# Kernel tuning notes

Hardware: AMD Instinct MI355X
Metric: run time of the kernel (lower is better)

Reference implementation:

```python
import jax, jax.numpy as jnp
import numpy as np

T, H, I, E, K = 4096, 2048, 1408, 8, 2  # tokens, hidden, intermediate, experts, top_k


def setup_inputs() -> dict:
    key = jax.random.key(0)
    ks = jax.random.split(key, 6)
    hidden_states = jax.random.normal(ks[0], (T, H), dtype=jnp.float32)
    gate_weight = jax.random.normal(ks[1], (E, H), dtype=jnp.float32) * 0.02  # fp32 gate, per source assert
    w13_weight = jax.random.randint(ks[2], (E, 2 * I, H), -127, 128, dtype=jnp.int8)
    w13_weight_scale = jax.random.uniform(ks[3], (E, 2 * I), dtype=jnp.float32, minval=0.5, maxval=1.5) * 0.005
    w2_weight = jax.random.randint(ks[4], (E, H, I), -127, 128, dtype=jnp.int8)
    w2_weight_scale = jax.random.uniform(ks[5], (E, H), dtype=jnp.float32, minval=0.5, maxval=1.5) * 0.005
    return dict(hidden_states=hidden_states, gate_weight=gate_weight,
                w13_weight=w13_weight, w13_weight_scale=w13_weight_scale,
                w2_weight=w2_weight, w2_weight_scale=w2_weight_scale)


def _dynamic_quant_i8(x):
    # per-token dynamic symmetric int8: scale = max|x|/127 (smooth scales default to ones)
    s = jnp.maximum(jnp.max(jnp.abs(x), axis=-1, keepdims=True) / 127.0, 1e-8)
    q = jnp.clip(jnp.round(x / s), -127.0, 127.0)
    return q, s


def reference(hidden_states, gate_weight, w13_weight, w13_weight_scale, w2_weight, w2_weight_scale):
    # --- gating: fp32 linear + topk softmax (renormalize=True) ---
    logits = hidden_states @ gate_weight.T              # [T, E]
    probs = jax.nn.softmax(logits, axis=-1)
    topv, topi = jax.lax.top_k(probs, K)                # [T, K]
    gates = topv / jnp.sum(topv, axis=-1, keepdims=True)
    # dense routing weights [T, E]: gate value where expert selected, else 0
    route = jnp.zeros((T, E), hidden_states.dtype).at[jnp.arange(T)[:, None], topi].add(gates)

    # --- dynamic per-token int8 quant of routed input (same token value for each of its K copies) ---
    q_in, s_in = _dynamic_quant_i8(hidden_states)       # [T, H], [T, 1]

    # --- grouped w8a8 GEMM (fc1) -> SwiGLU -> requant -> grouped GEMM (fc2) -> weighted combine ---
    def step(acc, xs):
        w13, s13, w2, s2w, r = xs                       # per-expert weights / route column [T]
        h1 = (q_in @ w13.T.astype(jnp.float32)) * s_in * s13[None, :]   # dequant fc1: [T, 2I]
        g, u = h1[:, :I], h1[:, I:]
        act = jax.nn.silu(g) * u                        # SwiGLU
        q_a, s_a = _dynamic_quant_i8(act)
        h2 = (q_a @ w2.T.astype(jnp.float32)) * s_a * s2w[None, :]      # dequant fc2: [T, H]
        return acc + r[:, None] * h2, None

    acc0 = jnp.zeros_like(hidden_states)
    out, _ = jax.lax.scan(step, acc0,
                          (w13_weight, w13_weight_scale, w2_weight, w2_weight_scale, route.T))
    return out
```

## Files before the change

kernel.cpp:

```cpp
#include <hip/hip_runtime.h>

#define T_TOK 4096
#define H_DIM 2048
#define I_DIM 1408
#define E_NUM 8
#define NI2   (2 * I_DIM)

typedef int v4i __attribute__((ext_vector_type(4)));

#define GLD_LDS16(gptr, lptr)                                                        \
  __builtin_amdgcn_global_load_lds(                                                  \
      (const __attribute__((address_space(1))) void*)(gptr),                         \
      (__attribute__((address_space(3))) void*)(lptr), 16, 0, 0)

__global__ __launch_bounds__(256) void pack_all(const int* __restrict__ w13,
                                                const int* __restrict__ w2,
                                                signed char* __restrict__ qw13,
                                                signed char* __restrict__ qw2,
                                                int n16a, int n16tot) {
  int i = blockIdx.x * 256 + threadIdx.x;
  if (i >= n16tot) return;
  const int* src;
  signed char* dst;
  int j;
  if (i < n16a) { src = w13; dst = qw13; j = i; }
  else          { src = w2;  dst = qw2;  j = i - n16a; }
  const int4* s4 = (const int4*)src + (size_t)j * 4;
  int4 v0 = s4[0], v1 = s4[1], v2 = s4[2], v3 = s4[3];
  union { signed char c[16]; int4 v; } pk;
  pk.c[0] = (signed char)v0.x;  pk.c[1] = (signed char)v0.y;
  pk.c[2] = (signed char)v0.z;  pk.c[3] = (signed char)v0.w;
  pk.c[4] = (signed char)v1.x;  pk.c[5] = (signed char)v1.y;
  pk.c[6] = (signed char)v1.z;  pk.c[7] = (signed char)v1.w;
  pk.c[8] = (signed char)v2.x;  pk.c[9] = (signed char)v2.y;
  pk.c[10] = (signed char)v2.z; pk.c[11] = (signed char)v2.w;
  pk.c[12] = (signed char)v3.x; pk.c[13] = (signed char)v3.y;
  pk.c[14] = (signed char)v3.z; pk.c[15] = (signed char)v3.w;
  ((int4*)dst)[j] = pk.v;
}

__global__ __launch_bounds__(256) void gate_route_quant(
    const float* __restrict__ hs, const float* __restrict__ gw,
    signed char* __restrict__ qin, float* __restrict__ s_in,
    int* __restrict__ tope, float* __restrict__ gts) {
  const int t = blockIdx.x;
  const int tid = threadIdx.x;
  const int lane = tid & 63;
  const int wave = tid >> 6;
  const float* row = hs + (size_t)t * H_DIM;

  const float4* r4 = (const float4*)row + tid * 2;
  float4 xa = r4[0], xb = r4[1];
  float x[8] = {xa.x, xa.y, xa.z, xa.w, xb.x, xb.y, xb.z, xb.w};

  double pd[8];
  for (int e = 0; e < 8; e++) pd[e] = 0.0;
  float am = 0.f;
  for (int j = 0; j < 8; j++) {
    float v = x[j];
    am = fmaxf(am, fabsf(v));
    int col = tid * 8 + j;
    for (int e = 0; e < 8; e++)
      pd[e] += (double)v * (double)gw[e * H_DIM + col];
  }
  for (int e = 0; e < 8; e++)
    for (int s = 32; s; s >>= 1) pd[e] += __shfl_down(pd[e], s);
  for (int s = 32; s; s >>= 1) am = fmaxf(am, __shfl_down(am, s));

  __shared__ double sred[4][8];
  __shared__ float sam[4];
  __shared__ float sbc;
  if (lane == 0) {
    for (int e = 0; e < 8; e++) sred[wave][e] = pd[e];
    sam[wave] = am;
  }
  __syncthreads();
  if (tid == 0) {
    float l[8];
    for (int e = 0; e < 8; e++)
      l[e] = (float)(sred[0][e] + sred[1][e] + sred[2][e] + sred[3][e]);
    float amx = fmaxf(fmaxf(sam[0], sam[1]), fmaxf(sam[2], sam[3]));
    float s = fmaxf(amx / 127.0f, 1e-8f);
    s_in[t] = s;
    sbc = s;
    int i1 = 0;
    for (int e = 1; e < 8; e++) if (l[e] > l[i1]) i1 = e;
    int i2 = -1;
    for (int e = 0; e < 8; e++) {
      if (e == i1) continue;
      if (i2 < 0 || l[e] > l[i2]) i2 = e;
    }
    float d = expf(l[i2] - l[i1]);
    tope[2 * t] = i1;     gts[2 * t] = 1.0f / (1.0f + d);
    tope[2 * t + 1] = i2; gts[2 * t + 1] = d / (1.0f + d);
  }
  __syncthreads();
  float s = sbc;
  union { signed char c[8]; unsigned long long u; } pk;
  for (int j = 0; j < 8; j++) {
    float q = rintf(x[j] / s);
    q = fminf(127.f, fmaxf(-127.f, q));
    pk.c[j] = (signed char)q;
  }
  ((unsigned long long*)(qin + (size_t)t * H_DIM))[tid] = pk.u;
}

__global__ __launch_bounds__(256) void build_lists(
    const int* __restrict__ tope, int* __restrict__ tok_list,
    int* __restrict__ epos, int* __restrict__ cnt) {
  const int e = blockIdx.x;
  const int tid = threadIdx.x;
  const int lane = tid & 63;
  const int wave = tid >> 6;
  __shared__ int wsum[4];
  __shared__ int base_s;
  if (tid == 0) base_s = 0;
  __syncthreads();
  for (int t0 = 0; t0 < T_TOK; t0 += 256) {
    int t = t0 + tid;
    int i1 = tope[2 * t], i2 = tope[2 * t + 1];
    int slot = (i1 == e) ? 0 : ((i2 == e) ? 1 : -1);
    unsigned long long m = __ballot(slot >= 0);
    int wpre = __popcll(m & ((1ull << lane) - 1ull));
    if (lane == 0) wsum[wave] = __popcll(m);
    __syncthreads();
    int pre = wpre;
    for (int w = 0; w < wave; w++) pre += wsum[w];
    int total = wsum[0] + wsum[1] + wsum[2] + wsum[3];
    int b = base_s;
    if (slot >= 0) {
      int pos = b + pre;
      tok_list[e * T_TOK + pos] = t;
      epos[2 * t + slot] = (e << 16) | pos;
    }
    __syncthreads();
    if (tid == 0) base_s = b + total;
  }
  __syncthreads();
  if (tid == 0) cnt[e] = base_s;
}

__global__ void calc_off(const int* __restrict__ cnt, int* __restrict__ off) {
  if (threadIdx.x == 0) {
    int s = 0;
    for (int e = 0; e < E_NUM; e++) { off[e] = s; s += cnt[e]; }
  }
}

__global__ __launch_bounds__(256, 3) void gemm1_silu(
    const signed char* __restrict__ qw13, const signed char* __restrict__ qin,
    const float* __restrict__ s_in, const float* __restrict__ s13,
    const int* __restrict__ tok_list, const int* __restrict__ cnt,
    const int* __restrict__ off, float* __restrict__ act,
    unsigned int* __restrict__ amax) {
  const int e = blockIdx.z;
  const int ce = cnt[e];
  const int m0 = blockIdx.y * 64;
  if (m0 >= ce) return;
  const int n0 = blockIdx.x * 128;

  __shared__ __align__(16) signed char As[64 * 64];
  __shared__ __align__(16) signed char Bg[128 * 64];
  __shared__ __align__(16) signed char Bu[128 * 64];

  const int tid = threadIdx.x;
  const int lane = tid & 63;
  const int wave = tid >> 6;
  const int quad = lane >> 4;
  const int ln = lane & 15;

  const int* tl = tok_list + e * T_TOK;
  const int rowA = tid >> 2;
  const int kc = (tid & 3) * 16;

  const int tA = tl[min(m0 + rowA, ce - 1)];
  const signed char* gA = qin + (size_t)tA * H_DIM + kc;
  const signed char* w13e = qw13 + (size_t)e * NI2 * H_DIM;
  const signed char* gBg0 = w13e + (size_t)(n0 + rowA) * H_DIM + kc;
  const signed char* gBg1 = w13e + (size_t)(n0 + rowA + 64) * H_DIM + kc;
  const signed char* gBu0 = gBg0 + (size_t)I_DIM * H_DIM;
  const signed char* gBu1 = gBg1 + (size_t)I_DIM * H_DIM;
  const int ldsA = tid * 16;
  const int lds1 = 4096 + ldsA;

  v4i accg[4][2], accu[4][2];
  v4i zero = {0, 0, 0, 0};
#pragma unroll
  for (int i = 0; i < 4; i++)
#pragma unroll
    for (int j = 0; j < 2; j++) { accg[i][j] = zero; accu[i][j] = zero; }

  for (int k0 = 0; k0 < H_DIM; k0 += 64) {
    __syncthreads();
    GLD_LDS16(gA + k0, As + ldsA);
    GLD_LDS16(gBg0 + k0, Bg + ldsA);
    GLD_LDS16(gBg1 + k0, Bg + lds1);
    GLD_LDS16(gBu0 + k0, Bu + ldsA);
    GLD_LDS16(gBu1 + k0, Bu + lds1);
    __syncthreads();

    v4i af[4], bgf[2], buf_[2];
#pragma unroll
    for (int mt = 0; mt < 4; mt++)
      af[mt] = *(const v4i*)(As + (mt * 16 + ln) * 64 + quad * 16);
#pragma unroll
    for (int nt = 0; nt < 2; nt++) {
      bgf[nt] = *(const v4i*)(Bg + (wave * 32 + nt * 16 + ln) * 64 + quad * 16);
      buf_[nt] = *(const v4i*)(Bu + (wave * 32 + nt * 16 + ln) * 64 + quad * 16);
    }
#pragma unroll
    for (int mt = 0; mt < 4; mt++)
#pragma unroll
      for (int nt = 0; nt < 2; nt++) {
        accg[mt][nt] = __builtin_amdgcn_mfma_i32_16x16x64_i8(af[mt], bgf[nt], accg[mt][nt], 0, 0, 0);
        accu[mt][nt] = __builtin_amdgcn_mfma_i32_16x16x64_i8(af[mt], buf_[nt], accu[mt][nt], 0, 0, 0);
      }
  }

  const float* s13e = s13 + e * NI2;
  float sg[2], su[2];
  int ncol[2];
#pragma unroll
  for (int nt = 0; nt < 2; nt++) {
    int n = n0 + wave * 32 + nt * 16 + ln;
    ncol[nt] = n;
    sg[nt] = s13e[n];
    su[nt] = s13e[I_DIM + n];
  }
  const int offe = off[e];
#pragma unroll
  for (int mt = 0; mt < 4; mt++) {
#pragma unroll
    for (int r = 0; r < 4; r++) {
      int mrel = m0 + mt * 16 + quad * 4 + r;
      bool valid = mrel < ce;
      int tok = tl[valid ? mrel : 0];
      float si = s_in[tok];
      int crow = offe + mrel;
      float* arow = act + (size_t)crow * I_DIM;
      float am = 0.f;
#pragma unroll
      for (int nt = 0; nt < 2; nt++) {
        float g = (float)accg[mt][nt][r] * si * sg[nt];
        float u = (float)accu[mt][nt][r] * si * su[nt];
        float a = g / (1.0f + expf(-g)) * u;
        if (valid) arow[ncol[nt]] = a;
        am = fmaxf(am, fabsf(a));
      }
      for (int s = 1; s < 16; s <<= 1) am = fmaxf(am, __shfl_xor(am, s, 16));
      if (valid && ln == 0) atomicMax(amax + crow, __float_as_uint(am));
    }
  }
}

__global__ __launch_bounds__(256) void quant_act(const float* __restrict__ act,
                                                 const unsigned int* __restrict__ amax,
                                                 signed char* __restrict__ qa,
                                                 float* __restrict__ s_a) {
  const int r = blockIdx.x;
  float am = __uint_as_float(amax[r]);
  float s = fmaxf(am / 127.0f, 1e-8f);
  if (threadIdx.x == 0) s_a[r] = s;
  const float* arow = act + (size_t)r * I_DIM;
  signed char* qrow = qa + (size_t)r * I_DIM;
  for (int j = threadIdx.x; j < I_DIM; j += 256) {
    float q = rintf(arow[j] / s);
    q = fminf(127.f, fmaxf(-127.f, q));
    qrow[j] = (signed char)q;
  }
}

__global__ __launch_bounds__(256, 4) void gemm2_h2(
    const signed char* __restrict__ qw2, const signed char* __restrict__ qa,
    const float* __restrict__ s_a, const float* __restrict__ s2w,
    const int* __restrict__ cnt, const int* __restrict__ off,
    float* __restrict__ h2s) {
  const int e = blockIdx.z;
  const int ce = cnt[e];
  const int m0 = blockIdx.y * 64;
  if (m0 >= ce) return;
  const int n0 = blockIdx.x * 128;
  const int offe = off[e];

  __shared__ __align__(16) signed char As[64 * 64];
  __shared__ __align__(16) signed char Bs[128 * 64];

  const int tid = threadIdx.x;
  const int lane = tid & 63;
  const int wave = tid >> 6;
  const int quad = lane >> 4;
  const int ln = lane & 15;

  const int rowA = tid >> 2;
  const int kc = (tid & 3) * 16;

  const signed char* gA = qa + (size_t)(offe + min(m0 + rowA, ce - 1)) * I_DIM + kc;
  const signed char* w2e = qw2 + (size_t)e * H_DIM * I_DIM;
  const signed char* gB0 = w2e + (size_t)(n0 + rowA) * I_DIM + kc;
  const signed char* gB1 = w2e + (size_t)(n0 + rowA + 64) * I_DIM + kc;
  const int ldsA = tid * 16;
  const int lds1 = 4096 + ldsA;

  v4i acc[4][2];
  v4i zero = {0, 0, 0, 0};
#pragma unroll
  for (int i = 0; i < 4; i++)
#pragma unroll
    for (int j = 0; j < 2; j++) acc[i][j] = zero;

  for (int k0 = 0; k0 < I_DIM; k0 += 64) {
    __syncthreads();
    GLD_LDS16(gA + k0, As + ldsA);
    GLD_LDS16(gB0 + k0, Bs + ldsA);
    GLD_LDS16(gB1 + k0, Bs + lds1);
    __syncthreads();

    v4i af[4], bf[2];
#pragma unroll
    for (int mt = 0; mt < 4; mt++)
      af[mt] = *(const v4i*)(As + (mt * 16 + ln) * 64 + quad * 16);
#pragma unroll
    for (int nt = 0; nt < 2; nt++)
      bf[nt] = *(const v4i*)(Bs + (wave * 32 + nt * 16 + ln) * 64 + quad * 16);
#pragma unroll
    for (int mt = 0; mt < 4; mt++)
#pragma unroll
      for (int nt = 0; nt < 2; nt++)
        acc[mt][nt] = __builtin_amdgcn_mfma_i32_16x16x64_i8(af[mt], bf[nt], acc[mt][nt], 0, 0, 0);
  }

  const float* s2e = s2w + e * H_DIM;
  float sw[2];
  int ncol[2];
#pragma unroll
  for (int nt = 0; nt < 2; nt++) {
    int n = n0 + wave * 32 + nt * 16 + ln;
    ncol[nt] = n;
    sw[nt] = s2e[n];
  }
#pragma unroll
  for (int mt = 0; mt < 4; mt++) {
#pragma unroll
    for (int r = 0; r < 4; r++) {
      int mrel = m0 + mt * 16 + quad * 4 + r;
      if (mrel >= ce) continue;
      float sa = s_a[offe + mrel];
      float* orow = h2s + (size_t)(offe + mrel) * H_DIM;
#pragma unroll
      for (int nt = 0; nt < 2; nt++)
        orow[ncol[nt]] = (float)acc[mt][nt][r] * sa * sw[nt];
    }
  }
}

__global__ __launch_bounds__(256) void gather_out(
    const float* __restrict__ h2s, const int* __restrict__ epos,
    const float* __restrict__ gts, const int* __restrict__ off,
    float* __restrict__ out) {
  const int t = blockIdx.x;
  int a = epos[2 * t], b = epos[2 * t + 1];
  float g1 = gts[2 * t], g2 = gts[2 * t + 1];
  int r1 = off[a >> 16] + (a & 0xffff);
  int r2 = off[b >> 16] + (b & 0xffff);
  const float4* R1 = (const float4*)(h2s + (size_t)r1 * H_DIM);
  const float4* R2 = (const float4*)(h2s + (size_t)r2 * H_DIM);
  float4* O = (float4*)(out + (size_t)t * H_DIM);
  for (int c = threadIdx.x; c < H_DIM / 4; c += 256) {
    float4 x = R1[c], y = R2[c];
    float4 z;
    z.x = g1 * x.x + g2 * y.x;
    z.y = g1 * x.y + g2 * y.y;
    z.z = g1 * x.z + g2 * y.z;
    z.w = g1 * x.w + g2 * y.w;
    O[c] = z;
  }
}

extern "C" void kernel_launch(void* const* d_in, const int* in_sizes, int n_in,
                              void* d_out, int out_size, void* d_ws, size_t ws_size,
                              hipStream_t stream) {
  const float* hs = (const float*)d_in[0];
  const float* gw = (const float*)d_in[1];
  const int* w13 = (const int*)d_in[2];
  const float* s13 = (const float*)d_in[3];
  const int* w2 = (const int*)d_in[4];
  const float* s2w = (const float*)d_in[5];
  float* out = (float*)d_out;

  char* ws = (char*)d_ws;
  size_t o = 0;
  auto take = [&](size_t b) {
    char* p = ws + o;
    o += (b + 255) & ~(size_t)255;
    return p;
  };
  signed char* qw13 = (signed char*)take((size_t)E_NUM * NI2 * H_DIM);
  signed char* qin = (signed char*)take((size_t)T_TOK * H_DIM);
  float* act = (float*)take((size_t)T_TOK * 2 * I_DIM * 4);
  float* h2s = (float*)qw13;
  signed char* qw2 = (signed char*)take((size_t)E_NUM * H_DIM * I_DIM);
  signed char* qa = (signed char*)take((size_t)T_TOK * 2 * I_DIM);
  float* sin_ = (float*)take((size_t)T_TOK * 4);
  float* sa = (float*)take((size_t)T_TOK * 2 * 4);
  unsigned int* amax = (unsigned int*)take((size_t)T_TOK * 2 * 4);
  int* tokl = (int*)take((size_t)E_NUM * T_TOK * 4);
  int* tope = (int*)take((size_t)T_TOK * 2 * 4);
  int* epos = (int*)take((size_t)T_TOK * 2 * 4);
  float* gts = (float*)take((size_t)T_TOK * 2 * 4);
  int* cnt = (int*)take(E_NUM * 4);
  int* off = (int*)take(E_NUM * 4);

  hipMemsetAsync(amax, 0, (size_t)T_TOK * 2 * 4, stream);

  {
    int n16a = E_NUM * NI2 * H_DIM / 16;
    int n16b = E_NUM * H_DIM * I_DIM / 16;
    int n16tot = n16a + n16b;
    pack_all<<<(n16tot + 255) / 256, 256, 0, stream>>>(w13, w2, qw13, qw2, n16a, n16tot);
  }
  gate_route_quant<<<T_TOK, 256, 0, stream>>>(hs, gw, qin, sin_, tope, gts);
  build_lists<<<E_NUM, 256, 0, stream>>>(tope, tokl, epos, cnt);
  calc_off<<<1, 64, 0, stream>>>(cnt, off);
  {
    dim3 g(I_DIM / 128, T_TOK / 64, E_NUM);
    gemm1_silu<<<g, 256, 0, stream>>>(qw13, qin, sin_, s13, tokl, cnt, off, act, amax);
  }
  quant_act<<<T_TOK * 2, 256, 0, stream>>>(act, amax, qa, sa);
  {
    dim3 g(H_DIM / 128, T_TOK / 64, E_NUM);
    gemm2_h2<<<g, 256, 0, stream>>>(qw2, qa, sa, s2w, cnt, off, h2s);
  }
  gather_out<<<T_TOK, 256, 0, stream>>>(h2s, epos, gts, off, out);
}
```

Before: 582.4 us.

## Double-buffer GEMM LDS tiles, swizzle LDS, widen gemm2 tile, parallelize list build

Both grouped GEMMs now double-buffer their LDS tiles, so the next k-slice's global-to-LDS loads are issued before the MFMAs on the current slice. Both also use an XOR swizzle on the LDS k-chunk to reduce bank conflicts. gemm2's N tile grows to 256 with a 4x4 accumulator set. Both GEMMs use a flattened 1D grid with the expert index in the low bits to interleave experts. build_lists now runs across 16 blocks using shared-memory and global atomics, with cnt cleared by a memset. This trades more LDS and registers per block, which may lower occupancy, and makes token order within each expert list nondeterministic.

```diff
diff --git a/kernel.cpp b/kernel.cpp
--- a/kernel.cpp
+++ b/kernel.cpp
@@ -108,36 +108,24 @@
 __global__ __launch_bounds__(256) void build_lists(
     const int* __restrict__ tope, int* __restrict__ tok_list,
     int* __restrict__ epos, int* __restrict__ cnt) {
-  const int e = blockIdx.x;
+  __shared__ int lc[E_NUM];
+  __shared__ int lbase[E_NUM];
   const int tid = threadIdx.x;
-  const int lane = tid & 63;
-  const int wave = tid >> 6;
-  __shared__ int wsum[4];
-  __shared__ int base_s;
-  if (tid == 0) base_s = 0;
-  __syncthreads();
-  for (int t0 = 0; t0 < T_TOK; t0 += 256) {
-    int t = t0 + tid;
-    int i1 = tope[2 * t], i2 = tope[2 * t + 1];
-    int slot = (i1 == e) ? 0 : ((i2 == e) ? 1 : -1);
-    unsigned long long m = __ballot(slot >= 0);
-    int wpre = __popcll(m & ((1ull << lane) - 1ull));
-    if (lane == 0) wsum[wave] = __popcll(m);
-    __syncthreads();
-    int pre = wpre;
-    for (int w = 0; w < wave; w++) pre += wsum[w];
-    int total = wsum[0] + wsum[1] + wsum[2] + wsum[3];
-    int b = base_s;
-    if (slot >= 0) {
-      int pos = b + pre;
-      tok_list[e * T_TOK + pos] = t;
-      epos[2 * t + slot] = (e << 16) | pos;
-    }
-    __syncthreads();
-    if (tid == 0) base_s = b + total;
-  }
-  __syncthreads();
-  if (tid == 0) cnt[e] = base_s;
+  if (tid < E_NUM) lc[tid] = 0;
+  __syncthreads();
+  const int t = blockIdx.x * 256 + tid;
+  int e0 = tope[2 * t], e1 = tope[2 * t + 1];
+  int p0 = atomicAdd(&lc[e0], 1);
+  int p1 = atomicAdd(&lc[e1], 1);
+  __syncthreads();
+  if (tid < E_NUM) lbase[tid] = atomicAdd(&cnt[tid], lc[tid]);
+  __syncthreads();
+  int pos0 = lbase[e0] + p0;
+  int pos1 = lbase[e1] + p1;
+  tok_list[e0 * T_TOK + pos0] = t;
+  tok_list[e1 * T_TOK + pos1] = t;
+  epos[2 * t] = (e0 << 16) | pos0;
+  epos[2 * t + 1] = (e1 << 16) | pos1;
 }
 
 __global__ void calc_off(const int* __restrict__ cnt, int* __restrict__ off) {
@@ -153,15 +141,18 @@
     const int* __restrict__ tok_list, const int* __restrict__ cnt,
     const int* __restrict__ off, float* __restrict__ act,
     unsigned int* __restrict__ amax) {
-  const int e = blockIdx.z;
+  const int bid = blockIdx.x;
+  const int e = bid & 7;
+  const int xt = bid >> 9;
+  const int yt = (bid >> 3) & 63;
   const int ce = cnt[e];
-  const int m0 = blockIdx.y * 64;
+  const int m0 = yt * 64;
   if (m0 >= ce) return;
-  const int n0 = blockIdx.x * 128;
-
-  __shared__ __align__(16) signed char As[64 * 64];
-  __shared__ __align__(16) signed char Bg[128 * 64];
-  __shared__ __align__(16) signed char Bu[128 * 64];
+  const int n0 = xt * 128;
+
+  __shared__ __align__(16) signed char As[2][64 * 64];
+  __shared__ __align__(16) signed char Bg[2][128 * 64];
+  __shared__ __align__(16) signed char Bu[2][128 * 64];
 
   const int tid = threadIdx.x;
   const int lane = tid & 63;
@@ -171,7 +162,7 @@
 
   const int* tl = tok_list + e * T_TOK;
   const int rowA = tid >> 2;
-  const int kc = (tid & 3) * 16;
+  const int kc = (((tid & 3) ^ (rowA & 3)) * 16);
 
   const int tA = tl[min(m0 + rowA, ce - 1)];
   const signed char* gA = qin + (size_t)tA * H_DIM + kc;
@@ -182,6 +173,7 @@
   const signed char* gBu1 = gBg1 + (size_t)I_DIM * H_DIM;
   const int ldsA = tid * 16;
   const int lds1 = 4096 + ldsA;
+  const int ks = ((quad ^ (ln & 3)) * 16);
 
   v4i accg[4][2], accu[4][2];
   v4i zero = {0, 0, 0, 0};
@@ -190,23 +182,32 @@
 #pragma unroll
     for (int j = 0; j < 2; j++) { accg[i][j] = zero; accu[i][j] = zero; }
 
-  for (int k0 = 0; k0 < H_DIM; k0 += 64) {
-    __syncthreads();
-    GLD_LDS16(gA + k0, As + ldsA);
-    GLD_LDS16(gBg0 + k0, Bg + ldsA);
-    GLD_LDS16(gBg1 + k0, Bg + lds1);
-    GLD_LDS16(gBu0 + k0, Bu + ldsA);
-    GLD_LDS16(gBu1 + k0, Bu + lds1);
-    __syncthreads();
-
+  GLD_LDS16(gA, &As[0][ldsA]);
+  GLD_LDS16(gBg0, &Bg[0][ldsA]);
+  GLD_LDS16(gBg1, &Bg[0][lds1]);
+  GLD_LDS16(gBu0, &Bu[0][ldsA]);
+  GLD_LDS16(gBu1, &Bu[0][lds1]);
+  __syncthreads();
+
+  const int NK = H_DIM / 64;
+  for (int kk = 0; kk < NK; ++kk) {
+    const int cur = kk & 1;
+    if (kk + 1 < NK) {
+      const int k0 = (kk + 1) * 64;
+      GLD_LDS16(gA + k0, &As[cur ^ 1][ldsA]);
+      GLD_LDS16(gBg0 + k0, &Bg[cur ^ 1][ldsA]);
+      GLD_LDS16(gBg1 + k0, &Bg[cur ^ 1][lds1]);
+      GLD_LDS16(gBu0 + k0, &Bu[cur ^ 1][ldsA]);
+      GLD_LDS16(gBu1 + k0, &Bu[cur ^ 1][lds1]);
+    }
     v4i af[4], bgf[2], buf_[2];
 #pragma unroll
     for (int mt = 0; mt < 4; mt++)
-      af[mt] = *(const v4i*)(As + (mt * 16 + ln) * 64 + quad * 16);
+      af[mt] = *(const v4i*)(&As[cur][(mt * 16 + ln) * 64 + ks]);
 #pragma unroll
     for (int nt = 0; nt < 2; nt++) {
-      bgf[nt] = *(const v4i*)(Bg + (wave * 32 + nt * 16 + ln) * 64 + quad * 16);
-      buf_[nt] = *(const v4i*)(Bu + (wave * 32 + nt * 16 + ln) * 64 + quad * 16);
+      bgf[nt] = *(const v4i*)(&Bg[cur][(wave * 32 + nt * 16 + ln) * 64 + ks]);
+      buf_[nt] = *(const v4i*)(&Bu[cur][(wave * 32 + nt * 16 + ln) * 64 + ks]);
     }
 #pragma unroll
     for (int mt = 0; mt < 4; mt++)
@@ -215,6 +216,7 @@
         accg[mt][nt] = __builtin_amdgcn_mfma_i32_16x16x64_i8(af[mt], bgf[nt], accg[mt][nt], 0, 0, 0);
         accu[mt][nt] = __builtin_amdgcn_mfma_i32_16x16x64_i8(af[mt], buf_[nt], accu[mt][nt], 0, 0, 0);
       }
+    __syncthreads();
   }
 
   const float* s13e = s13 + e * NI2;
@@ -270,20 +272,23 @@
   }
 }
 
-__global__ __launch_bounds__(256, 4) void gemm2_h2(
+__global__ __launch_bounds__(256, 3) void gemm2_h2(
     const signed char* __restrict__ qw2, const signed char* __restrict__ qa,
     const float* __restrict__ s_a, const float* __restrict__ s2w,
     const int* __restrict__ cnt, const int* __restrict__ off,
     float* __restrict__ h2s) {
-  const int e = blockIdx.z;
+  const int bid = blockIdx.x;
+  const int e = bid & 7;
+  const int xt = bid >> 9;
+  const int yt = (bid >> 3) & 63;
   const int ce = cnt[e];
-  const int m0 = blockIdx.y * 64;
+  const int m0 = yt * 64;
   if (m0 >= ce) return;
-  const int n0 = blockIdx.x * 128;
+  const int n0 = xt * 256;
   const int offe = off[e];
 
-  __shared__ __align__(16) signed char As[64 * 64];
-  __shared__ __align__(16) signed char Bs[128 * 64];
+  __shared__ __align__(16) signed char As[2][64 * 64];
+  __shared__ __align__(16) signed char Bs[2][256 * 64];
 
   const int tid = threadIdx.x;
   const int lane = tid & 63;
@@ -292,49 +297,63 @@
   const int ln = lane & 15;
 
   const int rowA = tid >> 2;
-  const int kc = (tid & 3) * 16;
+  const int kc = (((tid & 3) ^ (rowA & 3)) * 16);
 
   const signed char* gA = qa + (size_t)(offe + min(m0 + rowA, ce - 1)) * I_DIM + kc;
   const signed char* w2e = qw2 + (size_t)e * H_DIM * I_DIM;
   const signed char* gB0 = w2e + (size_t)(n0 + rowA) * I_DIM + kc;
-  const signed char* gB1 = w2e + (size_t)(n0 + rowA + 64) * I_DIM + kc;
+  const signed char* gB1 = gB0 + (size_t)64 * I_DIM;
+  const signed char* gB2 = gB0 + (size_t)128 * I_DIM;
+  const signed char* gB3 = gB0 + (size_t)192 * I_DIM;
   const int ldsA = tid * 16;
-  const int lds1 = 4096 + ldsA;
-
-  v4i acc[4][2];
+  const int ks = ((quad ^ (ln & 3)) * 16);
+
+  v4i acc[4][4];
   v4i zero = {0, 0, 0, 0};
 #pragma unroll
   for (int i = 0; i < 4; i++)
 #pragma unroll
-    for (int j = 0; j < 2; j++) acc[i][j] = zero;
-
-  for (int k0 = 0; k0 < I_DIM; k0 += 64) {
+    for (int j = 0; j < 4; j++) acc[i][j] = zero;
+
+  GLD_LDS16(gA, &As[0][ldsA]);
+  GLD_LDS16(gB0, &Bs[0][ldsA]);
+  GLD_LDS16(gB1, &Bs[0][4096 + ldsA]);
+  GLD_LDS16(gB2, &Bs[0][8192 + ldsA]);
+  GLD_LDS16(gB3, &Bs[0][12288 + ldsA]);
+  __syncthreads();
+
+  const int NK = I_DIM / 64;
+  for (int kk = 0; kk < NK; ++kk) {
+    const int cur = kk & 1;
+    if (kk + 1 < NK) {
+      const int k0 = (kk + 1) * 64;
+      GLD_LDS16(gA + k0, &As[cur ^ 1][ldsA]);
+      GLD_LDS16(gB0 + k0, &Bs[cur ^ 1][ldsA]);
+      GLD_LDS16(gB1 + k0, &Bs[cur ^ 1][4096 + ldsA]);
+      GLD_LDS16(gB2 + k0, &Bs[cur ^ 1][8192 + ldsA]);
+      GLD_LDS16(gB3 + k0, &Bs[cur ^ 1][12288 + ldsA]);
+    }
+    v4i af[4], bf[4];
+#pragma unroll
+    for (int mt = 0; mt < 4; mt++)
+      af[mt] = *(const v4i*)(&As[cur][(mt * 16 + ln) * 64 + ks]);
+#pragma unroll
+    for (int nt = 0; nt < 4; nt++)
+      bf[nt] = *(const v4i*)(&Bs[cur][(wave * 64 + nt * 16 + ln) * 64 + ks]);
+#pragma unroll
+    for (int mt = 0; mt < 4; mt++)
+#pragma unroll
+      for (int nt = 0; nt < 4; nt++)
+        acc[mt][nt] = __builtin_amdgcn_mfma_i32_16x16x64_i8(af[mt], bf[nt], acc[mt][nt], 0, 0, 0);
     __syncthreads();
-    GLD_LDS16(gA + k0, As + ldsA);
-    GLD_LDS16(gB0 + k0, Bs + ldsA);
-    GLD_LDS16(gB1 + k0, Bs + lds1);
-    __syncthreads();
-
-    v4i af[4], bf[2];
-#pragma unroll
-    for (int mt = 0; mt < 4; mt++)
-      af[mt] = *(const v4i*)(As + (mt * 16 + ln) * 64 + quad * 16);
-#pragma unroll
-    for (int nt = 0; nt < 2; nt++)
-      bf[nt] = *(const v4i*)(Bs + (wave * 32 + nt * 16 + ln) * 64 + quad * 16);
-#pragma unroll
-    for (int mt = 0; mt < 4; mt++)
-#pragma unroll
-      for (int nt = 0; nt < 2; nt++)
-        acc[mt][nt] = __builtin_amdgcn_mfma_i32_16x16x64_i8(af[mt], bf[nt], acc[mt][nt], 0, 0, 0);
   }
 
   const float* s2e = s2w + e * H_DIM;
-  float sw[2];
-  int ncol[2];
-#pragma unroll
-  for (int nt = 0; nt < 2; nt++) {
-    int n = n0 + wave * 32 + nt * 16 + ln;
+  float sw[4];
+  int ncol[4];
+#pragma unroll
+  for (int nt = 0; nt < 4; nt++) {
+    int n = n0 + wave * 64 + nt * 16 + ln;
     ncol[nt] = n;
     sw[nt] = s2e[n];
   }
@@ -347,7 +366,7 @@
       float sa = s_a[offe + mrel];
       float* orow = h2s + (size_t)(offe + mrel) * H_DIM;
 #pragma unroll
-      for (int nt = 0; nt < 2; nt++)
+      for (int nt = 0; nt < 4; nt++)
         orow[ncol[nt]] = (float)acc[mt][nt][r] * sa * sw[nt];
     }
   }
@@ -411,6 +430,7 @@
   int* off = (int*)take(E_NUM * 4);
 
   hipMemsetAsync(amax, 0, (size_t)T_TOK * 2 * 4, stream);
+  hipMemsetAsync(cnt, 0, (size_t)E_NUM * 4, stream);
 
   {
     int n16a = E_NUM * NI2 * H_DIM / 16;
@@ -419,16 +439,10 @@
     pack_all<<<(n16tot + 255) / 256, 256, 0, stream>>>(w13, w2, qw13, qw2, n16a, n16tot);
   }
   gate_route_quant<<<T_TOK, 256, 0, stream>>>(hs, gw, qin, sin_, tope, gts);
-  build_lists<<<E_NUM, 256, 0, stream>>>(tope, tokl, epos, cnt);
+  build_lists<<<T_TOK / 256, 256, 0, stream>>>(tope, tokl, epos, cnt);
   calc_off<<<1, 64, 0, stream>>>(cnt, off);
-  {
-    dim3 g(I_DIM / 128, T_TOK / 64, E_NUM);
-    gemm1_silu<<<g, 256, 0, stream>>>(qw13, qin, sin_, s13, tokl, cnt, off, act, amax);
-  }
+  gemm1_silu<<<(I_DIM / 128) * 64 * E_NUM, 256, 0, stream>>>(qw13, qin, sin_, s13, tokl, cnt, off, act, amax);
   quant_act<<<T_TOK * 2, 256, 0, stream>>>(act, amax, qa, sa);
-  {
-    dim3 g(H_DIM / 128, T_TOK / 64, E_NUM);
-    gemm2_h2<<<g, 256, 0, stream>>>(qw2, qa, sa, s2w, cnt, off, h2s);
-  }
+  gemm2_h2<<<(H_DIM / 256) * 64 * E_NUM, 256, 0, stream>>>(qw2, qa, sa, s2w, cnt, off, h2s);
   gather_out<<<T_TOK, 256, 0, stream>>>(h2s, epos, gts, off, out);
 }
```

Measured after the change: 604.8 us. +3.8%, slower.
